# Optimization experiments

Measured on AMD Instinct MI355X. Metric: run time of the kernel, lower is better.

## Reference

```python
import jax, jax.numpy as jnp
import numpy as np

H = 1024        # hidden_dim
MD = 2048       # memory_dim
L = 16384       # memory length == max_length
N = 8           # head_N
# sys.float_info.min underflows to 0.0 in float32, exactly as in the torch
# original (python float * float32 tensor). Kept for faithfulness.
TINY = jnp.float32(2.2250738585072014e-308)


def setup_inputs() -> dict:
    key = jax.random.key(0)
    ks = jax.random.split(key, 12)
    s_h = 1.0 / np.sqrt(H)
    s_m = 1.0 / np.sqrt(MD)
    s_o = 1.0 / np.sqrt(2 * H)
    return {
        "x": jax.random.normal(ks[0], (1, 1, H), jnp.float32),
        "memory": jax.random.normal(ks[1], (L, MD), jnp.float32),
        "Wq": jax.random.uniform(ks[2], (H, H), jnp.float32, -s_h, s_h),
        "bq": jax.random.uniform(ks[3], (H,), jnp.float32, -s_h, s_h),
        "Wk": jax.random.uniform(ks[4], (H, MD), jnp.float32, -s_m, s_m),
        "bk": jax.random.uniform(ks[5], (H,), jnp.float32, -s_m, s_m),
        "Wv": jax.random.uniform(ks[6], (H, MD), jnp.float32, -s_m, s_m),
        "bv": jax.random.uniform(ks[7], (H,), jnp.float32, -s_m, s_m),
        "Wo": jax.random.uniform(ks[8], (H, 2 * H), jnp.float32, -s_o, s_o),
        "bo": jax.random.uniform(ks[9], (H,), jnp.float32, -s_o, s_o),
    }


def reference(x, memory, Wq, bq, Wk, bk, Wv, bv, Wo, bo):
    d = H // N  # per-head dim
    # Q: (1,H) -> (1,d,N) -> (N,1,d), scaled by d**-0.5
    q = x.reshape(1, -1) @ Wq.T + bq
    Q = q.reshape(1, d, N).transpose(2, 0, 1) * (d ** -0.5)
    # K: (L,H) -> (L,d,N) -> (N,d,L)
    K = (memory @ Wk.T + bk).reshape(-1, d, N).transpose(2, 1, 0)
    QK = jnp.einsum('nod,ndl->nol', Q, K)  # (N,1,L)
    # pad mask: 1 where the memory row sums to zero, else 0 (as in torch nonzero-set)
    any_zero = memory.sum(axis=1)
    pad_mask = (any_zero == 0).astype(QK.dtype)[None, None, :]
    QK = QK + pad_mask * TINY
    attn = jax.nn.softmax(QK, axis=-1)
    # V: (L,H) -> (L,d,N) -> (N,L,d)
    V = (memory @ Wv.T + bv).reshape(-1, d, N).transpose(2, 0, 1)
    feat = jnp.einsum('nol,nld->nod', attn, V)      # (N,1,d)
    feat = feat.transpose(1, 2, 0).reshape(1, 1, H)  # (1,1,H)
    ax = jnp.concatenate([x, feat], axis=-1)         # (1,1,2H)
    return jax.nn.relu(ax @ Wo.T + bo)
```

## Files before the change

### kernel.cpp

```cpp
#include <hip/hip_runtime.h>
#include <math.h>

#define LROWS 16384
#define HDIM  1024
#define MDIM  2048
#define NH    8
#define RSQRT_D 0.08838834764831844f

#define OFF_W     0
#define OFF_BETA  16384
#define OFF_Z     16392
#define OFF_Q     16400
#define OFF_FEAT  17424
#define OFF_Y     18448
#define OFF_S2    34832
#define OFF_YBUF  296976

__device__ __forceinline__ float dot4(float4 a, float4 b) {
  return a.x * b.x + a.y * b.y + a.z * b.z + a.w * b.w;
}
__device__ __forceinline__ void fma4(float4& acc, float s, float4 v) {
  acc.x = fmaf(s, v.x, acc.x); acc.y = fmaf(s, v.y, acc.y);
  acc.z = fmaf(s, v.z, acc.z); acc.w = fmaf(s, v.w, acc.w);
}
__device__ __forceinline__ void add4(float4& a, float4 v) {
  a.x += v.x; a.y += v.y; a.z += v.z; a.w += v.w;
}

__global__ __launch_bounds__(256) void k1_q(const float* __restrict__ x,
                                            const float* __restrict__ Wq,
                                            const float* __restrict__ bq,
                                            const float* __restrict__ bk,
                                            float* __restrict__ ws) {
  int tid = threadIdx.x, lane = tid & 63;
  int j = blockIdx.x * 4 + (tid >> 6);
  const float4* xr = (const float4*)x;
  const float4* wr = (const float4*)(Wq + (size_t)j * HDIM);
  float acc = 0.f;
#pragma unroll
  for (int i = 0; i < 4; ++i) {
    int idx = i * 64 + lane;
    acc += dot4(xr[idx], wr[idx]);
  }
#pragma unroll
  for (int off = 32; off; off >>= 1) acc += __shfl_xor(acc, off);
  if (lane == 0) {
    float qj = acc + bq[j];
    ws[OFF_Q + j] = qj;
    atomicAdd(&ws[OFF_BETA + (j & 7)], qj * bk[j]);
  }
}

__global__ __launch_bounds__(256) void k2_w(const float* __restrict__ Wk,
                                            float* __restrict__ ws) {
  int tid = threadIdx.x;
  int mc = blockIdx.x & 7, cc = blockIdx.x >> 3;
  int m = mc * 256 + tid;
  const float* q = ws + OFF_Q;
  float acc[8];
#pragma unroll
  for (int n = 0; n < 8; ++n) acc[n] = 0.f;
  int c0 = cc * 32;
#pragma unroll
  for (int cb = 0; cb < 32; cb += 8) {
#pragma unroll
    for (int u = 0; u < 8; ++u)
      acc[u] = fmaf(q[c0 + cb + u], Wk[(size_t)(c0 + cb + u) * MDIM + m], acc[u]);
  }
#pragma unroll
  for (int n = 0; n < 8; ++n) atomicAdd(&ws[OFF_W + n * MDIM + m], acc[n]);
}

__global__ __launch_bounds__(256, 4) void kA2(const float* __restrict__ mem,
                                              float* __restrict__ ws) {
  __shared__ float4 wlds[2048];
  int tid = threadIdx.x, lane = tid & 63, wv = tid >> 6;
  int rg = blockIdx.x >> 1, ch = blockIdx.x & 1;
  int r0 = rg * 16;

  const float4* wsrc = (const float4*)(ws + OFF_W + ch * 1024);
#pragma unroll
  for (int k = 0; k < 8; ++k) {
    int qi = k * 256 + tid;
    int n = qi >> 8, c4 = qi & 255;
    wlds[qi] = wsrc[n * 512 + c4];
  }
  __syncthreads();

  float acc[4][8];
#pragma unroll
  for (int rr = 0; rr < 4; ++rr)
#pragma unroll
    for (int n = 0; n < 8; ++n) acc[rr][n] = 0.f;

  const size_t cbase = (size_t)ch * 1024;
  float4 mv[4], mvn[4];
#pragma unroll
  for (int rr = 0; rr < 4; ++rr)
    mv[rr] = *(const float4*)(mem + (size_t)(r0 + wv * 4 + rr) * MDIM + cbase + (size_t)lane * 4);

#pragma unroll
  for (int step = 0; step < 4; ++step) {
    int cq = step * 64 + lane;
    float4 wvv[8];
#pragma unroll
    for (int n = 0; n < 8; ++n) wvv[n] = wlds[n * 256 + cq];
    if (step < 3) {
#pragma unroll
      for (int rr = 0; rr < 4; ++rr)
        mvn[rr] = *(const float4*)(mem + (size_t)(r0 + wv * 4 + rr) * MDIM + cbase + (size_t)(cq + 64) * 4);
    }
#pragma unroll
    for (int rr = 0; rr < 4; ++rr) {
#pragma unroll
      for (int n = 0; n < 8; ++n) {
        acc[rr][n] = fmaf(mv[rr].x, wvv[n].x, acc[rr][n]);
        acc[rr][n] = fmaf(mv[rr].y, wvv[n].y, acc[rr][n]);
        acc[rr][n] = fmaf(mv[rr].z, wvv[n].z, acc[rr][n]);
        acc[rr][n] = fmaf(mv[rr].w, wvv[n].w, acc[rr][n]);
      }
    }
#pragma unroll
    for (int rr = 0; rr < 4; ++rr) mv[rr] = mvn[rr];
  }

#pragma unroll
  for (int off = 1; off < 64; off <<= 1) {
#pragma unroll
    for (int rr = 0; rr < 4; ++rr)
#pragma unroll
      for (int n = 0; n < 8; ++n)
        acc[rr][n] += __shfl_xor(acc[rr][n], off);
  }
  if (lane == 0) {
    float* sdst = ws + OFF_S2 + (size_t)ch * 131072 + (size_t)(r0 + wv * 4) * 8;
#pragma unroll
    for (int rr = 0; rr < 4; ++rr)
#pragma unroll
      for (int n = 0; n < 8; ++n)
        sdst[rr * 8 + n] = acc[rr][n];
  }
}

__global__ __launch_bounds__(256, 4) void kB2(const float* __restrict__ mem,
                                              float* __restrict__ ws) {
  __shared__ __align__(16) float pp[256];
  __shared__ float zz[32];
  int tid = threadIdx.x;
  int rc = blockIdx.x >> 1, ch = blockIdx.x & 1;
  int r0 = rc * 32;
  {
    int n = tid & 7;
    int r = r0 + (tid >> 3);
    float s0 = ws[OFF_S2 + (size_t)r * 8 + n];
    float s1 = ws[OFF_S2 + 131072 + (size_t)r * 8 + n];
    float p = __expf((s0 + s1 + ws[OFF_BETA + n]) * RSQRT_D);
    pp[tid] = p;
    if (ch == 0) {
      float z = p;
      z += __shfl_xor(z, 8); z += __shfl_xor(z, 16); z += __shfl_xor(z, 32);
      if ((tid & 63) < 8) zz[(tid >> 6) * 8 + n] = z;
    }
  }
  __syncthreads();
  if (ch == 0 && tid < 8)
    atomicAdd(&ws[OFF_Z + tid], zz[tid] + zz[8 + tid] + zz[16 + tid] + zz[24 + tid]);

  float4 acc[8];
#pragma unroll
  for (int n = 0; n < 8; ++n) acc[n] = make_float4(0.f, 0.f, 0.f, 0.f);

  const float* base = mem + (size_t)r0 * MDIM + ch * 1024 + tid * 4;
#pragma unroll 4
  for (int r = 0; r < 32; ++r) {
    float4 mv = *(const float4*)(base + (size_t)r * MDIM);
    float4 pA = *(const float4*)(pp + r * 8);
    float4 pB = *(const float4*)(pp + r * 8 + 4);
    fma4(acc[0], pA.x, mv); fma4(acc[1], pA.y, mv);
    fma4(acc[2], pA.z, mv); fma4(acc[3], pA.w, mv);
    fma4(acc[4], pB.x, mv); fma4(acc[5], pB.y, mv);
    fma4(acc[6], pB.z, mv); fma4(acc[7], pB.w, mv);
  }
  float* yb = ws + OFF_YBUF + (size_t)rc * 16384 + ch * 1024 + tid * 4;
#pragma unroll
  for (int n = 0; n < 8; ++n)
    *(float4*)(yb + n * MDIM) = acc[n];
}

__global__ __launch_bounds__(256) void k4c(float* __restrict__ ws) {
  __shared__ float4 sA[256];
  int t = threadIdx.x;
  int quad = blockIdx.x * 16 + (t & 15);
  int b0 = (t >> 4) * 32;
  const float4* src = (const float4*)(ws + OFF_YBUF);
  float4 acc = make_float4(0.f, 0.f, 0.f, 0.f);
  for (int b = b0; b < b0 + 32; ++b)
    add4(acc, src[(size_t)b * 4096 + quad]);
  sA[(t & 15) * 16 + (t >> 4)] = acc;
  __syncthreads();
  if (t < 16) {
    float4 s = sA[t * 16];
#pragma unroll
    for (int j = 1; j < 16; ++j) add4(s, sA[t * 16 + j]);
    ((float4*)(ws + OFF_Y))[blockIdx.x * 16 + t] = s;
  }
}

__global__ __launch_bounds__(256) void k6_feat(const float* __restrict__ Wv,
                                               const float* __restrict__ bv,
                                               float* __restrict__ ws) {
  int tid = threadIdx.x, lane = tid & 63;
  int c = blockIdx.x * 4 + (tid >> 6);
  int n = c & 7;
  const float4* yb = (const float4*)(ws + OFF_Y + n * MDIM);
  const float4* wb = (const float4*)(Wv + (size_t)c * MDIM);
  float acc = 0.f;
#pragma unroll
  for (int s = 0; s < 8; ++s) {
    int idx = s * 64 + lane;
    acc += dot4(yb[idx], wb[idx]);
  }
#pragma unroll
  for (int off = 32; off; off >>= 1) acc += __shfl_xor(acc, off);
  if (lane == 0) ws[OFF_FEAT + c] = acc / ws[OFF_Z + n] + bv[c];
}

__global__ __launch_bounds__(256) void k7_out(const float* __restrict__ x,
                                              const float* __restrict__ Wo,
                                              const float* __restrict__ bo,
                                              const float* __restrict__ ws,
                                              float* __restrict__ out) {
  int tid = threadIdx.x, lane = tid & 63;
  int j = blockIdx.x * 4 + (tid >> 6);
  const float4* wb = (const float4*)(Wo + (size_t)j * 2048);
  const float4* xr = (const float4*)x;
  const float4* fr = (const float4*)(ws + OFF_FEAT);
  float acc = 0.f;
#pragma unroll
  for (int s = 0; s < 4; ++s) {
    int idx = s * 64 + lane;
    acc += dot4(xr[idx], wb[idx]);
    acc += dot4(fr[idx], wb[256 + idx]);
  }
#pragma unroll
  for (int off = 32; off; off >>= 1) acc += __shfl_xor(acc, off);
  if (lane == 0) out[j] = fmaxf(acc + bo[j], 0.f);
}

extern "C" void kernel_launch(void* const* d_in, const int* in_sizes, int n_in,
                              void* d_out, int out_size, void* d_ws, size_t ws_size,
                              hipStream_t stream) {
  const float* x   = (const float*)d_in[0];
  const float* mem = (const float*)d_in[1];
  const float* Wq  = (const float*)d_in[2];
  const float* bq  = (const float*)d_in[3];
  const float* Wk  = (const float*)d_in[4];
  const float* bk  = (const float*)d_in[5];
  const float* Wv  = (const float*)d_in[6];
  const float* bv  = (const float*)d_in[7];
  const float* Wo  = (const float*)d_in[8];
  const float* bo  = (const float*)d_in[9];
  float* ws  = (float*)d_ws;
  float* out = (float*)d_out;

  hipMemsetAsync(ws, 0, OFF_Q * sizeof(float), stream);

  k1_q   <<<256, 256, 0, stream>>>(x, Wq, bq, bk, ws);
  k2_w   <<<256, 256, 0, stream>>>(Wk, ws);
  kA2    <<<2048, 256, 0, stream>>>(mem, ws);
  kB2    <<<1024, 256, 0, stream>>>(mem, ws);
  k4c    <<<256, 256, 0, stream>>>(ws);
  k6_feat<<<256, 256, 0, stream>>>(Wv, bv, ws);
  k7_out <<<256, 256, 0, stream>>>(x, Wo, bo, ws, out);
}
```

Before: 289.0 us.

## Fuse all stages into one cooperative persistent kernel with grid syncs

Replaces the seven separate kernel launches and the workspace memset with a single cooperative kernel of 1024 blocks that runs each stage in turn, separated by grid-wide barriers. Atomics are removed: Z partials and beta are now written deterministically and reduced in later phases, and the Wk projection is restructured per block. The aim is to remove launch gaps and memset overhead between the small phases. In exchange, grid-sync costs are added, the 32KB shared array may limit occupancy for the memory-bound phases, and if the cooperative launch fails there is a fallback path of separate kernels.

```diff
diff --git a/kernel.cpp b/kernel.cpp
--- a/kernel.cpp
+++ b/kernel.cpp
@@ -1,10 +1,12 @@
 #include <hip/hip_runtime.h>
+#include <hip/hip_cooperative_groups.h>
 #include <math.h>
+
+namespace cg = cooperative_groups;
 
 #define LROWS 16384
 #define HDIM  1024
 #define MDIM  2048
-#define NH    8
 #define RSQRT_D 0.08838834764831844f
 
 #define OFF_W     0
@@ -13,8 +15,9 @@
 #define OFF_Q     16400
 #define OFF_FEAT  17424
 #define OFF_Y     18448
-#define OFF_S2    34832
-#define OFF_YBUF  296976
+#define OFF_ZP    34832
+#define OFF_S2    38928
+#define OFF_YBUF  301072
 
 __device__ __forceinline__ float dot4(float4 a, float4 b) {
   return a.x * b.x + a.y * b.y + a.z * b.z + a.w * b.w;
@@ -27,128 +30,134 @@
   a.x += v.x; a.y += v.y; a.z += v.z; a.w += v.w;
 }
 
-__global__ __launch_bounds__(256) void k1_q(const float* __restrict__ x,
-                                            const float* __restrict__ Wq,
-                                            const float* __restrict__ bq,
-                                            const float* __restrict__ bk,
-                                            float* __restrict__ ws) {
-  int tid = threadIdx.x, lane = tid & 63;
-  int j = blockIdx.x * 4 + (tid >> 6);
-  const float4* xr = (const float4*)x;
-  const float4* wr = (const float4*)(Wq + (size_t)j * HDIM);
-  float acc = 0.f;
+__device__ __forceinline__ void p0_q(const float* __restrict__ x,
+                                     const float* __restrict__ Wq,
+                                     const float* __restrict__ bq,
+                                     float* __restrict__ ws,
+                                     float* lds, int bid, int tid) {
+  int lane = tid & 63, wv = tid >> 6;
+  const float4* x4 = (const float4*)x;
+  const float4* w4 = (const float4*)(Wq + (size_t)bid * HDIM);
+  float a = dot4(x4[tid], w4[tid]);
+#pragma unroll
+  for (int off = 32; off; off >>= 1) a += __shfl_xor(a, off);
+  if (lane == 0) lds[wv] = a;
+  __syncthreads();
+  if (tid == 0) ws[OFF_Q + bid] = lds[0] + lds[1] + lds[2] + lds[3] + bq[bid];
+}
+
+__device__ __forceinline__ void p1_w(const float* __restrict__ Wk,
+                                     const float* __restrict__ bk,
+                                     float* __restrict__ ws,
+                                     float* lds, int bid, int tid) {
+  int n = tid >> 5, g = tid & 31;
+  int m0 = bid * 2;
+  const float* q = ws + OFF_Q;
+  float ax = 0.f, ay = 0.f;
 #pragma unroll
   for (int i = 0; i < 4; ++i) {
-    int idx = i * 64 + lane;
-    acc += dot4(xr[idx], wr[idx]);
-  }
-#pragma unroll
-  for (int off = 32; off; off >>= 1) acc += __shfl_xor(acc, off);
-  if (lane == 0) {
-    float qj = acc + bq[j];
-    ws[OFF_Q + j] = qj;
-    atomicAdd(&ws[OFF_BETA + (j & 7)], qj * bk[j]);
-  }
-}
-
-__global__ __launch_bounds__(256) void k2_w(const float* __restrict__ Wk,
-                                            float* __restrict__ ws) {
-  int tid = threadIdx.x;
-  int mc = blockIdx.x & 7, cc = blockIdx.x >> 3;
-  int m = mc * 256 + tid;
-  const float* q = ws + OFF_Q;
-  float acc[8];
-#pragma unroll
-  for (int n = 0; n < 8; ++n) acc[n] = 0.f;
-  int c0 = cc * 32;
-#pragma unroll
-  for (int cb = 0; cb < 32; cb += 8) {
-#pragma unroll
-    for (int u = 0; u < 8; ++u)
-      acc[u] = fmaf(q[c0 + cb + u], Wk[(size_t)(c0 + cb + u) * MDIM + m], acc[u]);
-  }
-#pragma unroll
-  for (int n = 0; n < 8; ++n) atomicAdd(&ws[OFF_W + n * MDIM + m], acc[n]);
-}
-
-__global__ __launch_bounds__(256, 4) void kA2(const float* __restrict__ mem,
-                                              float* __restrict__ ws) {
-  __shared__ float4 wlds[2048];
-  int tid = threadIdx.x, lane = tid & 63, wv = tid >> 6;
-  int rg = blockIdx.x >> 1, ch = blockIdx.x & 1;
-  int r0 = rg * 16;
-
+    int c = 8 * (g + 32 * i) + n;
+    float2 wk = *(const float2*)(Wk + (size_t)c * MDIM + m0);
+    float qc = q[c];
+    ax = fmaf(qc, wk.x, ax);
+    ay = fmaf(qc, wk.y, ay);
+  }
+#pragma unroll
+  for (int off = 1; off < 32; off <<= 1) {
+    ax += __shfl_xor(ax, off);
+    ay += __shfl_xor(ay, off);
+  }
+  if (g == 0) *(float2*)(ws + OFF_W + n * MDIM + m0) = make_float2(ax, ay);
+  if (bid == 0) {
+    int nn = tid & 7;
+    float b = 0.f;
+#pragma unroll
+    for (int i = 0; i < 4; ++i) {
+      int c = tid + 256 * i;
+      b = fmaf(q[c], bk[c], b);
+    }
+    b += __shfl_xor(b, 8); b += __shfl_xor(b, 16); b += __shfl_xor(b, 32);
+    if ((tid & 63) < 8) lds[(tid >> 6) * 8 + nn] = b;
+    __syncthreads();
+    if (tid < 8)
+      ws[OFF_BETA + tid] = lds[tid] + lds[8 + tid] + lds[16 + tid] + lds[24 + tid];
+  }
+}
+
+__device__ __forceinline__ void p2_scores(const float* __restrict__ mem,
+                                          float* __restrict__ ws,
+                                          float* lds, int bid, int tid) {
+  int lane = tid & 63, wv = tid >> 6;
+  int ch = bid & 1, rg = bid >> 1;
+  float4* wlds = (float4*)lds;
   const float4* wsrc = (const float4*)(ws + OFF_W + ch * 1024);
 #pragma unroll
   for (int k = 0; k < 8; ++k) {
     int qi = k * 256 + tid;
-    int n = qi >> 8, c4 = qi & 255;
-    wlds[qi] = wsrc[n * 512 + c4];
-  }
-  __syncthreads();
-
-  float acc[4][8];
-#pragma unroll
-  for (int rr = 0; rr < 4; ++rr)
-#pragma unroll
-    for (int n = 0; n < 8; ++n) acc[rr][n] = 0.f;
-
-  const size_t cbase = (size_t)ch * 1024;
-  float4 mv[4], mvn[4];
-#pragma unroll
-  for (int rr = 0; rr < 4; ++rr)
-    mv[rr] = *(const float4*)(mem + (size_t)(r0 + wv * 4 + rr) * MDIM + cbase + (size_t)lane * 4);
-
-#pragma unroll
-  for (int step = 0; step < 4; ++step) {
-    int cq = step * 64 + lane;
-    float4 wvv[8];
-#pragma unroll
-    for (int n = 0; n < 8; ++n) wvv[n] = wlds[n * 256 + cq];
-    if (step < 3) {
+    wlds[qi] = wsrc[(qi >> 8) * 512 + (qi & 255)];
+  }
+  __syncthreads();
+#pragma unroll
+  for (int pass = 0; pass < 2; ++pass) {
+    int r0 = rg * 32 + pass * 16 + wv * 4;
+    const float* base = mem + (size_t)r0 * MDIM + ch * 1024;
+    float acc[4][8];
+#pragma unroll
+    for (int rr = 0; rr < 4; ++rr)
+#pragma unroll
+      for (int n = 0; n < 8; ++n) acc[rr][n] = 0.f;
+    float4 mv[4], mvn[4];
+#pragma unroll
+    for (int rr = 0; rr < 4; ++rr)
+      mv[rr] = *(const float4*)(base + rr * MDIM + lane * 4);
+#pragma unroll
+    for (int step = 0; step < 4; ++step) {
+      int cq = step * 64 + lane;
+      if (step < 3) {
+#pragma unroll
+        for (int rr = 0; rr < 4; ++rr)
+          mvn[rr] = *(const float4*)(base + rr * MDIM + (cq + 64) * 4);
+      }
+#pragma unroll
+      for (int n = 0; n < 8; ++n) {
+        float4 wv4 = wlds[n * 256 + cq];
+#pragma unroll
+        for (int rr = 0; rr < 4; ++rr) {
+          acc[rr][n] = fmaf(mv[rr].x, wv4.x, acc[rr][n]);
+          acc[rr][n] = fmaf(mv[rr].y, wv4.y, acc[rr][n]);
+          acc[rr][n] = fmaf(mv[rr].z, wv4.z, acc[rr][n]);
+          acc[rr][n] = fmaf(mv[rr].w, wv4.w, acc[rr][n]);
+        }
+      }
+#pragma unroll
+      for (int rr = 0; rr < 4; ++rr) mv[rr] = mvn[rr];
+    }
+#pragma unroll
+    for (int off = 1; off < 64; off <<= 1)
 #pragma unroll
       for (int rr = 0; rr < 4; ++rr)
-        mvn[rr] = *(const float4*)(mem + (size_t)(r0 + wv * 4 + rr) * MDIM + cbase + (size_t)(cq + 64) * 4);
+#pragma unroll
+        for (int n = 0; n < 8; ++n)
+          acc[rr][n] += __shfl_xor(acc[rr][n], off);
+    if (lane == 0) {
+      float* sdst = ws + OFF_S2 + (size_t)ch * 131072 + (size_t)r0 * 8;
+#pragma unroll
+      for (int rr = 0; rr < 4; ++rr)
+#pragma unroll
+        for (int n = 0; n < 8; ++n)
+          sdst[rr * 8 + n] = acc[rr][n];
     }
-#pragma unroll
-    for (int rr = 0; rr < 4; ++rr) {
-#pragma unroll
-      for (int n = 0; n < 8; ++n) {
-        acc[rr][n] = fmaf(mv[rr].x, wvv[n].x, acc[rr][n]);
-        acc[rr][n] = fmaf(mv[rr].y, wvv[n].y, acc[rr][n]);
-        acc[rr][n] = fmaf(mv[rr].z, wvv[n].z, acc[rr][n]);
-        acc[rr][n] = fmaf(mv[rr].w, wvv[n].w, acc[rr][n]);
-      }
-    }
-#pragma unroll
-    for (int rr = 0; rr < 4; ++rr) mv[rr] = mvn[rr];
-  }
-
-#pragma unroll
-  for (int off = 1; off < 64; off <<= 1) {
-#pragma unroll
-    for (int rr = 0; rr < 4; ++rr)
-#pragma unroll
-      for (int n = 0; n < 8; ++n)
-        acc[rr][n] += __shfl_xor(acc[rr][n], off);
-  }
-  if (lane == 0) {
-    float* sdst = ws + OFF_S2 + (size_t)ch * 131072 + (size_t)(r0 + wv * 4) * 8;
-#pragma unroll
-    for (int rr = 0; rr < 4; ++rr)
-#pragma unroll
-      for (int n = 0; n < 8; ++n)
-        sdst[rr * 8 + n] = acc[rr][n];
-  }
-}
-
-__global__ __launch_bounds__(256, 4) void kB2(const float* __restrict__ mem,
-                                              float* __restrict__ ws) {
-  __shared__ __align__(16) float pp[256];
-  __shared__ float zz[32];
-  int tid = threadIdx.x;
-  int rc = blockIdx.x >> 1, ch = blockIdx.x & 1;
+  }
+}
+
+__device__ __forceinline__ void p3_wsum(const float* __restrict__ mem,
+                                        float* __restrict__ ws,
+                                        float* lds, int bid, int tid) {
+  int lane = tid & 63, wv = tid >> 6;
+  int ch = bid & 1, rc = bid >> 1;
   int r0 = rc * 32;
+  float* pp = lds;
+  float* zz = lds + 256;
   {
     int n = tid & 7;
     int r = r0 + (tid >> 3);
@@ -159,23 +168,22 @@
     if (ch == 0) {
       float z = p;
       z += __shfl_xor(z, 8); z += __shfl_xor(z, 16); z += __shfl_xor(z, 32);
-      if ((tid & 63) < 8) zz[(tid >> 6) * 8 + n] = z;
+      if (lane < 8) zz[wv * 8 + lane] = z;
     }
   }
   __syncthreads();
   if (ch == 0 && tid < 8)
-    atomicAdd(&ws[OFF_Z + tid], zz[tid] + zz[8 + tid] + zz[16 + tid] + zz[24 + tid]);
+    ws[OFF_ZP + rc * 8 + tid] = zz[tid] + zz[8 + tid] + zz[16 + tid] + zz[24 + tid];
 
   float4 acc[8];
 #pragma unroll
   for (int n = 0; n < 8; ++n) acc[n] = make_float4(0.f, 0.f, 0.f, 0.f);
-
   const float* base = mem + (size_t)r0 * MDIM + ch * 1024 + tid * 4;
+  const float4* pp4 = (const float4*)pp;
 #pragma unroll 4
   for (int r = 0; r < 32; ++r) {
     float4 mv = *(const float4*)(base + (size_t)r * MDIM);
-    float4 pA = *(const float4*)(pp + r * 8);
-    float4 pB = *(const float4*)(pp + r * 8 + 4);
+    float4 pA = pp4[r * 2], pB = pp4[r * 2 + 1];
     fma4(acc[0], pA.x, mv); fma4(acc[1], pA.y, mv);
     fma4(acc[2], pA.z, mv); fma4(acc[3], pA.w, mv);
     fma4(acc[4], pB.x, mv); fma4(acc[5], pB.y, mv);
@@ -187,64 +195,142 @@
     *(float4*)(yb + n * MDIM) = acc[n];
 }
 
-__global__ __launch_bounds__(256) void k4c(float* __restrict__ ws) {
-  __shared__ float4 sA[256];
-  int t = threadIdx.x;
-  int quad = blockIdx.x * 16 + (t & 15);
-  int b0 = (t >> 4) * 32;
+__device__ __forceinline__ void p4_yred(float* __restrict__ ws,
+                                        float* lds, int bid, int tid) {
+  int lane = tid & 63, wv = tid >> 6;
   const float4* src = (const float4*)(ws + OFF_YBUF);
-  float4 acc = make_float4(0.f, 0.f, 0.f, 0.f);
-  for (int b = b0; b < b0 + 32; ++b)
-    add4(acc, src[(size_t)b * 4096 + quad]);
-  sA[(t & 15) * 16 + (t >> 4)] = acc;
-  __syncthreads();
-  if (t < 16) {
-    float4 s = sA[t * 16];
-#pragma unroll
-    for (int j = 1; j < 16; ++j) add4(s, sA[t * 16 + j]);
-    ((float4*)(ws + OFF_Y))[blockIdx.x * 16 + t] = s;
-  }
-}
-
-__global__ __launch_bounds__(256) void k6_feat(const float* __restrict__ Wv,
-                                               const float* __restrict__ bv,
-                                               float* __restrict__ ws) {
-  int tid = threadIdx.x, lane = tid & 63;
-  int c = blockIdx.x * 4 + (tid >> 6);
-  int n = c & 7;
+  int qd = bid * 4 + (tid & 3);
+  int h = tid >> 2;
+  float4 a = make_float4(0.f, 0.f, 0.f, 0.f);
+#pragma unroll
+  for (int i = 0; i < 8; ++i)
+    add4(a, src[(size_t)(h + 64 * i) * 4096 + qd]);
+#pragma unroll
+  for (int off = 4; off < 64; off <<= 1) {
+    a.x += __shfl_xor(a.x, off);
+    a.y += __shfl_xor(a.y, off);
+    a.z += __shfl_xor(a.z, off);
+    a.w += __shfl_xor(a.w, off);
+  }
+  float4* sq = (float4*)lds;
+  if (lane < 4) sq[wv * 4 + lane] = a;
+  __syncthreads();
+  if (tid < 4) {
+    float4 s = sq[tid];
+    add4(s, sq[4 + tid]); add4(s, sq[8 + tid]); add4(s, sq[12 + tid]);
+    ((float4*)(ws + OFF_Y))[bid * 4 + tid] = s;
+  }
+  if (bid == 0) {
+    int n = tid & 7;
+    float z = 0.f;
+#pragma unroll
+    for (int i = 0; i < 16; ++i)
+      z += ws[OFF_ZP + ((tid >> 3) + 32 * i) * 8 + n];
+    z += __shfl_xor(z, 8); z += __shfl_xor(z, 16); z += __shfl_xor(z, 32);
+    float* zzz = lds + 64;
+    if (lane < 8) zzz[wv * 8 + lane] = z;
+    __syncthreads();
+    if (tid < 8)
+      ws[OFF_Z + tid] = zzz[tid] + zzz[8 + tid] + zzz[16 + tid] + zzz[24 + tid];
+  }
+}
+
+__device__ __forceinline__ void p5_feat(const float* __restrict__ Wv,
+                                        const float* __restrict__ bv,
+                                        float* __restrict__ ws,
+                                        float* lds, int bid, int tid) {
+  int lane = tid & 63, wv = tid >> 6;
+  int c = bid, n = c & 7;
   const float4* yb = (const float4*)(ws + OFF_Y + n * MDIM);
   const float4* wb = (const float4*)(Wv + (size_t)c * MDIM);
-  float acc = 0.f;
-#pragma unroll
-  for (int s = 0; s < 8; ++s) {
-    int idx = s * 64 + lane;
-    acc += dot4(yb[idx], wb[idx]);
-  }
-#pragma unroll
-  for (int off = 32; off; off >>= 1) acc += __shfl_xor(acc, off);
-  if (lane == 0) ws[OFF_FEAT + c] = acc / ws[OFF_Z + n] + bv[c];
-}
-
-__global__ __launch_bounds__(256) void k7_out(const float* __restrict__ x,
-                                              const float* __restrict__ Wo,
-                                              const float* __restrict__ bo,
-                                              const float* __restrict__ ws,
-                                              float* __restrict__ out) {
-  int tid = threadIdx.x, lane = tid & 63;
-  int j = blockIdx.x * 4 + (tid >> 6);
+  float a = dot4(yb[tid], wb[tid]) + dot4(yb[tid + 256], wb[tid + 256]);
+#pragma unroll
+  for (int off = 32; off; off >>= 1) a += __shfl_xor(a, off);
+  if (lane == 0) lds[wv] = a;
+  __syncthreads();
+  if (tid == 0)
+    ws[OFF_FEAT + c] = (lds[0] + lds[1] + lds[2] + lds[3]) / ws[OFF_Z + n] + bv[c];
+}
+
+__device__ __forceinline__ void p6_out(const float* __restrict__ x,
+                                       const float* __restrict__ Wo,
+                                       const float* __restrict__ bo,
+                                       const float* __restrict__ ws,
+                                       float* __restrict__ out,
+                                       float* lds, int bid, int tid) {
+  int lane = tid & 63, wv = tid >> 6;
+  int j = bid;
   const float4* wb = (const float4*)(Wo + (size_t)j * 2048);
-  const float4* xr = (const float4*)x;
-  const float4* fr = (const float4*)(ws + OFF_FEAT);
-  float acc = 0.f;
-#pragma unroll
-  for (int s = 0; s < 4; ++s) {
-    int idx = s * 64 + lane;
-    acc += dot4(xr[idx], wb[idx]);
-    acc += dot4(fr[idx], wb[256 + idx]);
-  }
-#pragma unroll
-  for (int off = 32; off; off >>= 1) acc += __shfl_xor(acc, off);
-  if (lane == 0) out[j] = fmaxf(acc + bo[j], 0.f);
+  const float4* x4 = (const float4*)x;
+  const float4* f4 = (const float4*)(ws + OFF_FEAT);
+  float a = dot4(x4[tid], wb[tid]) + dot4(f4[tid], wb[256 + tid]);
+#pragma unroll
+  for (int off = 32; off; off >>= 1) a += __shfl_xor(a, off);
+  if (lane == 0) lds[wv] = a;
+  __syncthreads();
+  if (tid == 0)
+    out[j] = fmaxf(lds[0] + lds[1] + lds[2] + lds[3] + bo[j], 0.f);
+}
+
+__global__ __launch_bounds__(256, 4) void mega(const float* __restrict__ x,
+                                               const float* __restrict__ mem,
+                                               const float* __restrict__ Wq,
+                                               const float* __restrict__ bq,
+                                               const float* __restrict__ Wk,
+                                               const float* __restrict__ bk,
+                                               const float* __restrict__ Wv,
+                                               const float* __restrict__ bv,
+                                               const float* __restrict__ Wo,
+                                               const float* __restrict__ bo,
+                                               float* __restrict__ ws,
+                                               float* __restrict__ out) {
+  __shared__ __align__(16) float lds[8192];
+  cg::grid_group g = cg::this_grid();
+  int bid = blockIdx.x, tid = threadIdx.x;
+  p0_q(x, Wq, bq, ws, lds, bid, tid);
+  g.sync();
+  p1_w(Wk, bk, ws, lds, bid, tid);
+  g.sync();
+  p2_scores(mem, ws, lds, bid, tid);
+  g.sync();
+  p3_wsum(mem, ws, lds, bid, tid);
+  g.sync();
+  p4_yred(ws, lds, bid, tid);
+  g.sync();
+  p5_feat(Wv, bv, ws, lds, bid, tid);
+  g.sync();
+  p6_out(x, Wo, bo, ws, out, lds, bid, tid);
+}
+
+__global__ __launch_bounds__(256) void f0(const float* x, const float* Wq,
+                                          const float* bq, float* ws) {
+  __shared__ __align__(16) float lds[8];
+  p0_q(x, Wq, bq, ws, lds, blockIdx.x, threadIdx.x);
+}
+__global__ __launch_bounds__(256) void f1(const float* Wk, const float* bk, float* ws) {
+  __shared__ __align__(16) float lds[32];
+  p1_w(Wk, bk, ws, lds, blockIdx.x, threadIdx.x);
+}
+__global__ __launch_bounds__(256, 4) void f2(const float* mem, float* ws) {
+  __shared__ __align__(16) float lds[8192];
+  p2_scores(mem, ws, lds, blockIdx.x, threadIdx.x);
+}
+__global__ __launch_bounds__(256, 4) void f3(const float* mem, float* ws) {
+  __shared__ __align__(16) float lds[288];
+  p3_wsum(mem, ws, lds, blockIdx.x, threadIdx.x);
+}
+__global__ __launch_bounds__(256) void f4(float* ws) {
+  __shared__ __align__(16) float lds[96];
+  p4_yred(ws, lds, blockIdx.x, threadIdx.x);
+}
+__global__ __launch_bounds__(256) void f5(const float* Wv, const float* bv, float* ws) {
+  __shared__ __align__(16) float lds[8];
+  p5_feat(Wv, bv, ws, lds, blockIdx.x, threadIdx.x);
+}
+__global__ __launch_bounds__(256) void f6(const float* x, const float* Wo,
+                                          const float* bo, const float* ws, float* out) {
+  __shared__ __align__(16) float lds[8];
+  p6_out(x, Wo, bo, ws, out, lds, blockIdx.x, threadIdx.x);
 }
 
 extern "C" void kernel_launch(void* const* d_in, const int* in_sizes, int n_in,
@@ -263,13 +349,18 @@
   float* ws  = (float*)d_ws;
   float* out = (float*)d_out;
 
-  hipMemsetAsync(ws, 0, OFF_Q * sizeof(float), stream);
-
-  k1_q   <<<256, 256, 0, stream>>>(x, Wq, bq, bk, ws);
-  k2_w   <<<256, 256, 0, stream>>>(Wk, ws);
-  kA2    <<<2048, 256, 0, stream>>>(mem, ws);
-  kB2    <<<1024, 256, 0, stream>>>(mem, ws);
-  k4c    <<<256, 256, 0, stream>>>(ws);
-  k6_feat<<<256, 256, 0, stream>>>(Wv, bv, ws);
-  k7_out <<<256, 256, 0, stream>>>(x, Wo, bo, ws, out);
-}
+  void* args[12] = {(void*)&x, (void*)&mem, (void*)&Wq, (void*)&bq,
+                    (void*)&Wk, (void*)&bk, (void*)&Wv, (void*)&bv,
+                    (void*)&Wo, (void*)&bo, (void*)&ws, (void*)&out};
+  hipError_t err = hipLaunchCooperativeKernel(mega, dim3(1024), dim3(256),
+                                              args, 0, stream);
+  if (err != hipSuccess) {
+    f0<<<1024, 256, 0, stream>>>(x, Wq, bq, ws);
+    f1<<<1024, 256, 0, stream>>>(Wk, bk, ws);
+    f2<<<1024, 256, 0, stream>>>(mem, ws);
+    f3<<<1024, 256, 0, stream>>>(mem, ws);
+    f4<<<1024, 256, 0, stream>>>(ws);
+    f5<<<1024, 256, 0, stream>>>(Wv, bv, ws);
+    f6<<<1024, 256, 0, stream>>>(x, Wo, bo, ws, out);
+  }
+}
```

Measured after the change: 1.011 ms. 250% more time.
